# Optimization experiments

Hardware: AMD Instinct MI355X
Metric: run time of the kernel (lower is better)

## Reference

```python
import jax, jax.numpy as jnp
import numpy as np

H = 16  # n_heads


def _ln(x, g, b, eps=1e-5):
    m = x.mean(-1, keepdims=True)
    v = ((x - m) ** 2).mean(-1, keepdims=True)
    return (x - m) / jnp.sqrt(v + eps) * g + b


def setup_inputs() -> dict:
    key = jax.random.key(0)
    ks = jax.random.split(key, 10)
    b, lq, d, dff, L = 2, 1024, 1024, 4096, 4
    s = 0.02
    return {
        "x": jax.random.normal(ks[0], (b, lq, d), jnp.float32),
        "memory_bank": jax.random.normal(ks[1], (L, b, lq, d), jnp.float32),
        "attn_mask": jax.random.bernoulli(ks[2], 0.3, (b, lq, lq)),
        "ln1_g": jnp.ones((d,), jnp.float32),
        "ln1_b": jnp.zeros((d,), jnp.float32),
        "Wq": jax.random.normal(ks[3], (d, d), jnp.float32) * s,
        "Wk": jax.random.normal(ks[4], (d, d), jnp.float32) * s,
        "Wv": jax.random.normal(ks[5], (d, d), jnp.float32) * s,
        "Wo": jax.random.normal(ks[6], (d, d), jnp.float32) * s,
        "ln2_g": jnp.ones((d,), jnp.float32),
        "ln2_b": jnp.zeros((d,), jnp.float32),
        "W1": jax.random.normal(ks[7], (d, dff), jnp.float32) * s,
        "b1": jnp.zeros((dff,), jnp.float32),
        "W2": jax.random.normal(ks[8], (dff, d), jnp.float32) * s,
        "b2": jnp.zeros((d,), jnp.float32),
    }


def reference(x, memory_bank, attn_mask, ln1_g, ln1_b, Wq, Wk, Wv, Wo,
              ln2_g, ln2_b, W1, b1, W2, b2):
    # x: [b, lq, d]; memory_bank: [L, b, lk, d]; attn_mask: [b, lq, lk] bool (True = masked)
    b, lq, d = x.shape
    dh = d // H
    # preprocess_attn: LayerNorm (eval mode -> dropouts are identity)
    q = _ln(x, ln1_g, ln1_b)
    # grow memory bank with current normalized input
    mem = jnp.concatenate([memory_bank, q[None]], axis=0)  # [L+1, b, lk, d]
    L, _, lk, _ = mem.shape
    # projections (bias-free); key/value projected per layer then flattened over (L, lk)
    pq = (q @ Wq).reshape(b, lq, H, dh).transpose(0, 2, 1, 3) * (dh ** -0.5)  # [b,h,lq,dh]
    pk = (mem @ Wk).transpose(1, 0, 2, 3).reshape(b, L * lk, H, dh).transpose(0, 2, 1, 3)
    pv = (mem @ Wv).transpose(1, 0, 2, 3).reshape(b, L * lk, H, dh).transpose(0, 2, 1, 3)
    scores = jnp.einsum('bhqd,bhkd->bhqk', pq, pk)           # [b,h,lq,L*lk]
    scores = scores.reshape(b, H, lq, L, lk)
    scores = jnp.where(attn_mask[:, None, :, None, :], -jnp.inf, scores)
    attn = jax.nn.softmax(scores.reshape(b, H, lq, L * lk), axis=-1)
    ctx = jnp.einsum('bhqk,bhkd->bhqd', attn, pv)            # [b,h,lq,dh]
    ctx = ctx.transpose(0, 2, 1, 3).reshape(b, lq, d)
    attn_out = ctx @ Wo
    # postprocess_attn: residual add
    x2 = x + attn_out
    # FFN: LayerNorm -> Linear -> ReLU -> Linear -> residual
    f = _ln(x2, ln2_g, ln2_b)
    f = jax.nn.relu(f @ W1 + b1) @ W2 + b2
    out = x2 + f
    return (out, mem)
```

## Files before the change

### kernel.cpp

```cpp
#include <hip/hip_runtime.h>
#include <hip/hip_bf16.h>

typedef __attribute__((ext_vector_type(8))) __bf16 bf16x8;
typedef __attribute__((ext_vector_type(4))) __bf16 bf16x4;
typedef __attribute__((ext_vector_type(4))) float f32x4;

#define MFMA16(a, b, c) __builtin_amdgcn_mfma_f32_16x16x32_bf16((a), (b), (c), 0, 0, 0)
#define LOG2E 1.4426950408889634f

static __device__ __forceinline__ float exp2_fast(float x) {
    float r; asm("v_exp_f32 %0, %1" : "=v"(r) : "v"(x)); return r;
}

__device__ __forceinline__ void gll16(const void* g, void* l) {
    __builtin_amdgcn_global_load_lds((const __attribute__((address_space(1))) void*)g,
                                     (__attribute__((address_space(3))) void*)l,
                                     16, 0, 0);
}

__global__ __launch_bounds__(256) void prep_kernel(const float* __restrict__ bank,
                                                   float* __restrict__ mem_out,
                                                   __bf16* __restrict__ membf,
                                                   const float* __restrict__ x,
                                                   const float* __restrict__ g,
                                                   const float* __restrict__ bta,
                                                   float* __restrict__ q_out,
                                                   __bf16* __restrict__ qbf) {
    __shared__ float rs[4], rs2[4];
    int blk = blockIdx.x;
    if (blk < 2048) {
        int i = blk * 256 + threadIdx.x;
        const float4* i4 = (const float4*)bank;
        float4* o4 = (float4*)mem_out;
        for (; i < 2097152; i += 2048 * 256) {
            float4 v = i4[i];
            o4[i] = v;
            if (membf) {
                bf16x4 ob = {(__bf16)v.x, (__bf16)v.y, (__bf16)v.z, (__bf16)v.w};
                ((bf16x4*)membf)[i] = ob;
            }
        }
    } else {
        int row = blk - 2048;
        const float4 v = ((const float4*)(x + (size_t)row * 1024))[threadIdx.x];
        float s = v.x + v.y + v.z + v.w;
        float s2 = v.x * v.x + v.y * v.y + v.z * v.z + v.w * v.w;
#pragma unroll
        for (int off = 1; off < 64; off <<= 1) {
            s += __shfl_xor(s, off);
            s2 += __shfl_xor(s2, off);
        }
        int wv = threadIdx.x >> 6;
        if ((threadIdx.x & 63) == 0) { rs[wv] = s; rs2[wv] = s2; }
        __syncthreads();
        s = rs[0] + rs[1] + rs[2] + rs[3];
        s2 = rs2[0] + rs2[1] + rs2[2] + rs2[3];
        float mean = s * (1.0f / 1024.0f);
        float var = s2 * (1.0f / 1024.0f) - mean * mean;
        float rstd = rsqrtf(var + 1e-5f);
        float4 gg = ((const float4*)g)[threadIdx.x];
        float4 bb = ((const float4*)bta)[threadIdx.x];
        float4 o;
        o.x = (v.x - mean) * rstd * gg.x + bb.x;
        o.y = (v.y - mean) * rstd * gg.y + bb.y;
        o.z = (v.z - mean) * rstd * gg.z + bb.z;
        o.w = (v.w - mean) * rstd * gg.w + bb.w;
        ((float4*)(q_out + (size_t)row * 1024))[threadIdx.x] = o;
        if (qbf) {
            bf16x4 ob = {(__bf16)o.x, (__bf16)o.y, (__bf16)o.z, (__bf16)o.w};
            ((bf16x4*)(qbf + (size_t)row * 1024))[threadIdx.x] = ob;
        }
    }
}

__global__ __launch_bounds__(256) void ln_kernel(const float* __restrict__ x,
                                                 const float* __restrict__ g,
                                                 const float* __restrict__ bta,
                                                 __bf16* __restrict__ outb) {
    int row = blockIdx.x;
    const float4 v = ((const float4*)(x + (size_t)row * 1024))[threadIdx.x];
    float s = v.x + v.y + v.z + v.w;
    float s2 = v.x * v.x + v.y * v.y + v.z * v.z + v.w * v.w;
#pragma unroll
    for (int off = 1; off < 64; off <<= 1) {
        s += __shfl_xor(s, off);
        s2 += __shfl_xor(s2, off);
    }
    __shared__ float rs[4], rs2[4];
    int wv = threadIdx.x >> 6;
    if ((threadIdx.x & 63) == 0) { rs[wv] = s; rs2[wv] = s2; }
    __syncthreads();
    s = rs[0] + rs[1] + rs[2] + rs[3];
    s2 = rs2[0] + rs2[1] + rs2[2] + rs2[3];
    float mean = s * (1.0f / 1024.0f);
    float var = s2 * (1.0f / 1024.0f) - mean * mean;
    float rstd = rsqrtf(var + 1e-5f);
    float4 gg = ((const float4*)g)[threadIdx.x];
    float4 bb = ((const float4*)bta)[threadIdx.x];
    bf16x4 ob;
    ob[0] = (__bf16)((v.x - mean) * rstd * gg.x + bb.x);
    ob[1] = (__bf16)((v.y - mean) * rstd * gg.y + bb.y);
    ob[2] = (__bf16)((v.z - mean) * rstd * gg.z + bb.z);
    ob[3] = (__bf16)((v.w - mean) * rstd * gg.w + bb.w);
    ((bf16x4*)(outb + (size_t)row * 1024))[threadIdx.x] = ob;
}

__global__ __launch_bounds__(256) void comb_ln2(const float* __restrict__ pc0,
                                                const float* __restrict__ pc1,
                                                const float* __restrict__ x,
                                                const float* __restrict__ g,
                                                const float* __restrict__ bta,
                                                float* __restrict__ x2,
                                                __bf16* __restrict__ fln) {
    int row = blockIdx.x;
    int idx = row * 256 + threadIdx.x;
    float4 a = ((const float4*)pc0)[idx];
    float4 b = ((const float4*)pc1)[idx];
    float4 r = ((const float4*)x)[idx];
    float4 v;
    v.x = a.x + b.x + r.x;
    v.y = a.y + b.y + r.y;
    v.z = a.z + b.z + r.z;
    v.w = a.w + b.w + r.w;
    ((float4*)x2)[idx] = v;
    float s = v.x + v.y + v.z + v.w;
    float s2 = v.x * v.x + v.y * v.y + v.z * v.z + v.w * v.w;
#pragma unroll
    for (int off = 1; off < 64; off <<= 1) {
        s += __shfl_xor(s, off);
        s2 += __shfl_xor(s2, off);
    }
    __shared__ float rs[4], rs2[4];
    int wv = threadIdx.x >> 6;
    if ((threadIdx.x & 63) == 0) { rs[wv] = s; rs2[wv] = s2; }
    __syncthreads();
    s = rs[0] + rs[1] + rs[2] + rs[3];
    s2 = rs2[0] + rs2[1] + rs2[2] + rs2[3];
    float mean = s * (1.0f / 1024.0f);
    float var = s2 * (1.0f / 1024.0f) - mean * mean;
    float rstd = rsqrtf(var + 1e-5f);
    float4 gg = ((const float4*)g)[threadIdx.x];
    float4 bb = ((const float4*)bta)[threadIdx.x];
    bf16x4 ob;
    ob[0] = (__bf16)((v.x - mean) * rstd * gg.x + bb.x);
    ob[1] = (__bf16)((v.y - mean) * rstd * gg.y + bb.y);
    ob[2] = (__bf16)((v.z - mean) * rstd * gg.z + bb.z);
    ob[3] = (__bf16)((v.w - mean) * rstd * gg.w + bb.w);
    ((bf16x4*)(fln + (size_t)row * 1024))[threadIdx.x] = ob;
}

__device__ __forceinline__ void tr_body(const float* __restrict__ in, __bf16* __restrict__ out,
                                        int K, int N, int k0, int n0) {
    __shared__ float tile[32][33];
    int tx = threadIdx.x & 31, ty = threadIdx.x >> 5;
#pragma unroll
    for (int i = 0; i < 4; i++)
        tile[ty + i * 8][tx] = in[(size_t)(k0 + ty + i * 8) * N + n0 + tx];
    __syncthreads();
#pragma unroll
    for (int i = 0; i < 4; i++)
        out[(size_t)(n0 + ty + i * 8) * K + k0 + tx] = (__bf16)tile[tx][ty + i * 8];
}

__global__ __launch_bounds__(256) void tr_early(const float* __restrict__ Wq,
                                                const float* __restrict__ Wk,
                                                const float* __restrict__ Wv,
                                                __bf16* __restrict__ Wq_t,
                                                __bf16* __restrict__ Wkv_t) {
    int w = blockIdx.x;
    int sel = w >> 10, within = w & 1023;
    const float* in = (sel == 0) ? Wq : ((sel == 1) ? Wk : Wv);
    __bf16* out = (sel == 0) ? Wq_t : (Wkv_t + (size_t)(sel - 1) * 1048576);
    tr_body(in, out, 1024, 1024, (within >> 5) * 32, (within & 31) * 32);
}

__global__ __launch_bounds__(256) void tr_late(const float* __restrict__ Wo,
                                               const float* __restrict__ W1,
                                               const float* __restrict__ W2,
                                               __bf16* __restrict__ Wo_t,
                                               __bf16* __restrict__ W1_t,
                                               __bf16* __restrict__ W2_t) {
    int w = blockIdx.x;
    const float* in;
    __bf16* out;
    int K, N, k0, n0;
    if (w < 1024) {
        in = Wo; out = Wo_t; K = 1024; N = 1024; n0 = (w & 31) * 32; k0 = (w >> 5) * 32;
    } else if (w < 5120) {
        int v = w - 1024;
        in = W1; out = W1_t; K = 1024; N = 4096; n0 = (v & 127) * 32; k0 = (v >> 7) * 32;
    } else {
        int v = w - 5120;
        in = W2; out = W2_t; K = 4096; N = 1024; n0 = (v & 31) * 32; k0 = (v >> 5) * 32;
    }
    tr_body(in, out, K, N, k0, n0);
}

template <int EPI, bool ABF16>
__device__ __forceinline__ void gemm_core(const void* __restrict__ Av,
                                          const __bf16* __restrict__ Bt,
                                          void* __restrict__ Cout,
                                          const float* __restrict__ bias,
                                          const float* __restrict__ res,
                                          int N, int lda, int ldb, int klen,
                                          float scale, int bm, int bn) {
    constexpr int LDA = ABF16 ? 32 : 40;
    __shared__ __bf16 As[128 * LDA];
    __shared__ __bf16 Bs[128 * 32];

    int t = threadIdx.x;
    int lane = t & 63, wave = t >> 6;
    int wm = (wave >> 1) * 64, wn = (wave & 1) * 64;
    int l16 = lane & 15, l4 = lane >> 4;

    f32x4 acc[4][4];
#pragma unroll
    for (int m = 0; m < 4; m++)
#pragma unroll
        for (int n = 0; n < 4; n++) acc[m][n] = (f32x4){0.f, 0.f, 0.f, 0.f};

    int srow = t >> 2;
    int scol = (t & 3) * 8;
    int ar = t >> 1, ak = (t & 1) * 16;
    const __bf16* Ab = (const __bf16*)Av;
    const float* Af = (const float*)Av;

    for (int k0 = 0; k0 < klen; k0 += 32) {
        gll16(Bt + (size_t)(bn + srow) * ldb + (k0 + scol), &Bs[wave * 512]);
        gll16(Bt + (size_t)(bn + 64 + srow) * ldb + (k0 + scol), &Bs[2048 + wave * 512]);
        if constexpr (ABF16) {
            gll16(Ab + (size_t)(bm + srow) * lda + (k0 + scol), &As[wave * 512]);
            gll16(Ab + (size_t)(bm + 64 + srow) * lda + (k0 + scol), &As[2048 + wave * 512]);
        } else {
            const float* ap = Af + (size_t)(bm + ar) * lda + k0 + ak;
            float4 f0 = ((const float4*)ap)[0];
            float4 f1 = ((const float4*)ap)[1];
            float4 f2 = ((const float4*)ap)[2];
            float4 f3 = ((const float4*)ap)[3];
            float ta[16] = {f0.x, f0.y, f0.z, f0.w, f1.x, f1.y, f1.z, f1.w,
                            f2.x, f2.y, f2.z, f2.w, f3.x, f3.y, f3.z, f3.w};
            bf16x8 v0, v1;
#pragma unroll
            for (int j = 0; j < 8; j++) { v0[j] = (__bf16)ta[j]; v1[j] = (__bf16)ta[j + 8]; }
            *(bf16x8*)&As[ar * 40 + ak] = v0;
            *(bf16x8*)&As[ar * 40 + ak + 8] = v1;
        }
        __syncthreads();

        bf16x8 af[4], bfr[4];
#pragma unroll
        for (int m = 0; m < 4; m++) af[m] = *(const bf16x8*)&As[(wm + m * 16 + l16) * LDA + l4 * 8];
#pragma unroll
        for (int n = 0; n < 4; n++) bfr[n] = *(const bf16x8*)&Bs[(wn + n * 16 + l16) * 32 + l4 * 8];
#pragma unroll
        for (int m = 0; m < 4; m++)
#pragma unroll
            for (int n = 0; n < 4; n++) acc[m][n] = MFMA16(af[m], bfr[n], acc[m][n]);
        __syncthreads();
    }

#pragma unroll
    for (int m = 0; m < 4; m++) {
#pragma unroll
        for (int r = 0; r < 4; r++) {
            int row = bm + wm + m * 16 + l4 * 4 + r;
#pragma unroll
            for (int n = 0; n < 4; n++) {
                int col = bn + wn + n * 16 + l16;
                float c = acc[m][n][r];
                size_t idx = (size_t)row * N + col;
                if (EPI == 0) {
                    ((__bf16*)Cout)[idx] = (__bf16)(c * scale);
                } else if (EPI == 1) {
                    ((float*)Cout)[idx] = c + res[idx];
                } else if (EPI == 2) {
                    ((__bf16*)Cout)[idx] = (__bf16)fmaxf(c + bias[col], 0.0f);
                } else if (EPI == 3) {
                    ((float*)Cout)[idx] = c + bias[col] + res[idx];
                } else {
                    ((float*)Cout)[idx] = c;
                }
            }
        }
    }
}

template <int EPI, bool ABF16>
__global__ __launch_bounds__(256) void gemm_bt(const void* __restrict__ Av,
                                               const __bf16* __restrict__ Bt,
                                               void* __restrict__ Cout,
                                               const float* __restrict__ bias,
                                               const float* __restrict__ res,
                                               int N, int K, float scale, int nbx) {
    int q = gridDim.x >> 3;
    int swz = (blockIdx.x & 7) * q + (blockIdx.x >> 3);
    int bn = (swz % nbx) * 128;
    int bm = (swz / nbx) * 128;
    gemm_core<EPI, ABF16>(Av, Bt, Cout, bias, res, N, K, K, K, scale, bm, bn);
}

template <bool ABF16>
__global__ __launch_bounds__(256) void gemm_proj(const void* __restrict__ Akv,
                                                 const __bf16* __restrict__ Wkv_t,
                                                 __bf16* __restrict__ PKV,
                                                 const void* __restrict__ Aq,
                                                 const __bf16* __restrict__ Wq_t,
                                                 __bf16* __restrict__ Pq) {
    int q = gridDim.x >> 3;
    int swz = (blockIdx.x & 7) * q + (blockIdx.x >> 3);
    const void* A;
    const __bf16* B;
    __bf16* C;
    int N, bm, bn;
    float sc;
    if (swz < 1280) {
        A = Akv; B = Wkv_t; C = PKV; N = 2048; sc = 1.0f;
        bn = (swz & 15) * 128; bm = (swz >> 4) * 128;
    } else {
        int p = swz - 1280;
        A = Aq; B = Wq_t; C = Pq; N = 1024; sc = 0.125f * LOG2E;
        bn = (p & 7) * 128; bm = (p >> 3) * 128;
    }
    gemm_core<0, ABF16>(A, B, C, nullptr, nullptr, N, 1024, 1024, 1024, sc, bm, bn);
}

__global__ __launch_bounds__(256) void gemm_w2(const __bf16* __restrict__ h1,
                                               const __bf16* __restrict__ W2_t,
                                               float* __restrict__ pc0,
                                               float* __restrict__ pc1) {
    int q = gridDim.x >> 3;
    int swz = (blockIdx.x & 7) * q + (blockIdx.x >> 3);
    int half = swz >> 7;
    int p = swz & 127;
    int bn = (p & 7) * 128, bm = (p >> 3) * 128;
    int koff = half * 2048;
    gemm_core<4, true>(h1 + koff, W2_t + koff, half ? pc1 : pc0, nullptr, nullptr,
                       1024, 4096, 4096, 2048, 1.0f, bm, bn);
}

__global__ __launch_bounds__(256) void gemm_wo(const __bf16* __restrict__ ctx,
                                               const __bf16* __restrict__ Wo_t,
                                               float* __restrict__ pc0,
                                               float* __restrict__ pc1) {
    int q = gridDim.x >> 3;
    int swz = (blockIdx.x & 7) * q + (blockIdx.x >> 3);
    int half = swz >> 7;
    int p = swz & 127;
    int bn = (p & 7) * 128, bm = (p >> 3) * 128;
    int koff = half * 512;
    gemm_core<4, true>(ctx + koff, Wo_t + koff, half ? pc1 : pc0, nullptr, nullptr,
                       1024, 1024, 1024, 512, 1.0f, bm, bn);
}

__global__ __launch_bounds__(256) void comb_kernel(const float* __restrict__ pc0,
                                                   const float* __restrict__ pc1,
                                                   const float* __restrict__ bias,
                                                   const float* __restrict__ res,
                                                   float* __restrict__ out) {
    int i = blockIdx.x * 256 + threadIdx.x;
    float4 a = ((const float4*)pc0)[i];
    float4 b = ((const float4*)pc1)[i];
    float4 r = ((const float4*)res)[i];
    float4 o;
    o.x = a.x + b.x + r.x;
    o.y = a.y + b.y + r.y;
    o.z = a.z + b.z + r.z;
    o.w = a.w + b.w + r.w;
    if (bias) {
        float4 bb = ((const float4*)bias)[i & 255];
        o.x += bb.x; o.y += bb.y; o.z += bb.z; o.w += bb.w;
    }
    ((float4*)out)[i] = o;
}

#define CK 64
#define NCH4 20
__global__ __launch_bounds__(256, 5) void attn_part(const __bf16* __restrict__ Pq,
                                                    const __bf16* __restrict__ PKV,
                                                    const unsigned char* __restrict__ mask,
                                                    __bf16* __restrict__ pacc,
                                                    float* __restrict__ pl) {
    int bh = blockIdx.x;
    int b = bh >> 4, h = bh & 15;
    int rng = blockIdx.z;
    int wave = threadIdx.x >> 6, lane = threadIdx.x & 63;
    int l16 = lane & 15, l4 = lane >> 4;
    int q0 = blockIdx.y * 64 + wave * 16;

    __shared__ __bf16 Ks[64][72];
    __shared__ __bf16 Vt[64][72];
    __shared__ __bf16 Ps[4][16][72];

    const f32x4 fzero = {0.f, 0.f, 0.f, 0.f};

    bf16x8 qf[2];
    {
        const __bf16* pqrow = Pq + (size_t)(b * 1024 + q0 + l16) * 1024 + h * 64;
        qf[0] = *(const bf16x8*)(pqrow + l4 * 8);
        qf[1] = *(const bf16x8*)(pqrow + 32 + l4 * 8);
    }

    f32x4 accT[4];
#pragma unroll
    for (int n = 0; n < 4; n++) accT[n] = fzero;
    float lsum = 0.0f;

    const unsigned char* mrow_p = mask + (size_t)b * (1024u * 1024u) + (size_t)(q0 + l16) * 1024;

    int tl = threadIdx.x;
    int skey = tl >> 2;
    int sd0 = (tl & 3) << 4;
    int kgbase = rng * 1280;

    bf16x8 rk0, rk1, rv0, rv1;
    unsigned int mk[4], mkn[4];
    {
        int kg = kgbase + skey;
        int lidx = kg >> 10, i = kg & 1023;
        size_t off = ((size_t)(lidx * 2048 + b * 1024 + i) << 11) + h * 64 + sd0;
        rk0 = *(const bf16x8*)(PKV + off);
        rk1 = *(const bf16x8*)(PKV + off + 8);
        rv0 = *(const bf16x8*)(PKV + off + 1024);
        rv1 = *(const bf16x8*)(PKV + off + 1032);
        int kloc = kgbase & 1023;
#pragma unroll
        for (int tile = 0; tile < 4; tile++)
            mk[tile] = *(const unsigned int*)(mrow_p + kloc + tile * 16 + l4 * 4);
    }

    for (int t = 0; t < NCH4; t++) {
        *(bf16x8*)&Ks[skey][sd0] = rk0;
        *(bf16x8*)&Ks[skey][sd0 + 8] = rk1;
#pragma unroll
        for (int j = 0; j < 8; j++) {
            int row = sd0 + j;
            Vt[row][skey ^ ((row >> 3) << 3)] = rv0[j];
            int row2 = sd0 + 8 + j;
            Vt[row2][skey ^ ((row2 >> 3) << 3)] = rv1[j];
        }
        __syncthreads();

        if (t + 1 < NCH4) {
            int kg = kgbase + (t + 1) * CK + skey;
            int lidx = kg >> 10, i = kg & 1023;
            size_t off = ((size_t)(lidx * 2048 + b * 1024 + i) << 11) + h * 64 + sd0;
            rk0 = *(const bf16x8*)(PKV + off);
            rk1 = *(const bf16x8*)(PKV + off + 8);
            rv0 = *(const bf16x8*)(PKV + off + 1024);
            rv1 = *(const bf16x8*)(PKV + off + 1032);
            int kloc = (kgbase + (t + 1) * CK) & 1023;
#pragma unroll
            for (int tile = 0; tile < 4; tile++)
                mkn[tile] = *(const unsigned int*)(mrow_p + kloc + tile * 16 + l4 * 4);
        }

        f32x4 s[4];
        __builtin_amdgcn_s_setprio(1);
#pragma unroll
        for (int tile = 0; tile < 4; tile++) {
            bf16x8 ka = *(const bf16x8*)&Ks[tile * 16 + l16][l4 * 8];
            bf16x8 kb = *(const bf16x8*)&Ks[tile * 16 + l16][32 + l4 * 8];
            f32x4 sz = fzero;
            sz = MFMA16(ka, qf[0], sz);
            sz = MFMA16(kb, qf[1], sz);
            s[tile] = sz;
        }
        __builtin_amdgcn_s_setprio(0);

        float psum = 0.0f;
#pragma unroll
        for (int tile = 0; tile < 4; tile++) {
            bf16x4 pk_;
#pragma unroll
            for (int r = 0; r < 4; r++) {
                float e = exp2_fast(s[tile][r]);
                e = ((mk[tile] >> (r * 8)) & 255u) ? 0.0f : e;
                psum += e;
                pk_[r] = (__bf16)e;
            }
            *(bf16x4*)&Ps[wave][l16][tile * 16 + l4 * 4] = pk_;
        }
        lsum += psum;
#pragma unroll
        for (int tile = 0; tile < 4; tile++) mk[tile] = mkn[tile];

        __builtin_amdgcn_s_setprio(1);
#pragma unroll
        for (int kk = 0; kk < 2; kk++) {
            bf16x8 pf = *(const bf16x8*)&Ps[wave][l16][kk * 32 + l4 * 8];
#pragma unroll
            for (int n = 0; n < 4; n++) {
                int row = n * 16 + l16;
                int colblk = (kk * 32 + l4 * 8) ^ ((row >> 3) << 3);
                bf16x8 vf = *(const bf16x8*)&Vt[row][colblk];
                accT[n] = MFMA16(vf, pf, accT[n]);
            }
        }
        __builtin_amdgcn_s_setprio(0);
        __syncthreads();
    }

    lsum += __shfl_xor(lsum, 16);
    lsum += __shfl_xor(lsum, 32);

    size_t blk = ((size_t)(bh * 16 + blockIdx.y) * 4 + rng);
    __bf16* pa = pacc + blk * 4096 + (size_t)(wave * 16 + l16) * 64;
#pragma unroll
    for (int n = 0; n < 4; n++) {
        bf16x4 o;
#pragma unroll
        for (int r = 0; r < 4; r++) o[r] = (__bf16)accT[n][r];
        *(bf16x4*)&pa[n * 16 + l4 * 4] = o;
    }
    if (l4 == 0) pl[blk * 64 + wave * 16 + l16] = lsum;
}

__global__ __launch_bounds__(256) void attn_comb(const __bf16* __restrict__ pacc,
                                                 const float* __restrict__ pl,
                                                 __bf16* __restrict__ ctx) {
    int bh = blockIdx.x, qb = blockIdx.y;
    int b = bh >> 4, h = bh & 15;
    int q = threadIdx.x >> 2, d0 = (threadIdx.x & 3) * 16;
    float acc[16];
#pragma unroll
    for (int j = 0; j < 16; j++) acc[j] = 0.0f;
    float l = 0.0f;
    size_t blk0 = ((size_t)(bh * 16 + qb)) * 4;
#pragma unroll
    for (int rng = 0; rng < 4; rng++) {
        size_t base = (blk0 + rng) * 4096 + (size_t)q * 64 + d0;
        bf16x8 a0 = *(const bf16x8*)&pacc[base];
        bf16x8 a1 = *(const bf16x8*)&pacc[base + 8];
#pragma unroll
        for (int j = 0; j < 8; j++) {
            acc[j] += (float)a0[j];
            acc[8 + j] += (float)a1[j];
        }
        l += pl[(blk0 + rng) * 64 + q];
    }
    float inv = 1.0f / l;
    __bf16* crow = ctx + ((size_t)(b * 1024 + qb * 64 + q) << 10) + h * 64 + d0;
    bf16x8 o0, o1;
#pragma unroll
    for (int j = 0; j < 8; j++) {
        o0[j] = (__bf16)(acc[j] * inv);
        o1[j] = (__bf16)(acc[8 + j] * inv);
    }
    *(bf16x8*)crow = o0;
    *(bf16x8*)(crow + 8) = o1;
}

#define KHALF 2560
#define NCH 40
__global__ __launch_bounds__(512, 4) void attn_kernel(const __bf16* __restrict__ Pq,
                                                      const __bf16* __restrict__ PKV,
                                                      const unsigned char* __restrict__ mask,
                                                      __bf16* __restrict__ ctx) {
    int bh = blockIdx.x;
    int b = bh >> 4, h = bh & 15;
    int wave = threadIdx.x >> 6, lane = threadIdx.x & 63;
    int grp = wave >> 2, wv = wave & 3;
    int l16 = lane & 15, l4 = lane >> 4;
    int q0 = blockIdx.y * 64 + wv * 16;

    __shared__ __bf16 Ks[2][64][72];
    __shared__ __bf16 Vt[2][64][72];
    __shared__ __bf16 Ps[8][16][72];

    const f32x4 fzero = {0.f, 0.f, 0.f, 0.f};

    bf16x8 qf[2];
    {
        const __bf16* pqrow = Pq + (size_t)(b * 1024 + q0 + l16) * 1024 + h * 64;
        qf[0] = *(const bf16x8*)(pqrow + l4 * 8);
        qf[1] = *(const bf16x8*)(pqrow + 32 + l4 * 8);
    }

    f32x4 accT[4];
#pragma unroll
    for (int n = 0; n < 4; n++) accT[n] = fzero;
    float lsum = 0.0f;

    const unsigned char* mrow_p = mask + (size_t)b * (1024u * 1024u) + (size_t)(q0 + l16) * 1024;

    int tl = threadIdx.x & 255;
    int skey = tl >> 2;
    int sd0 = (tl & 3) << 4;
    int kgbase = grp * KHALF;

    bf16x8 rk0, rk1, rv0, rv1;
    unsigned int mk[4], mkn[4];
    {
        int kg = kgbase + skey;
        int lidx = kg >> 10, i = kg & 1023;
        size_t off = ((size_t)(lidx * 2048 + b * 1024 + i) << 11) + h * 64 + sd0;
        rk0 = *(const bf16x8*)(PKV + off);
        rk1 = *(const bf16x8*)(PKV + off + 8);
        rv0 = *(const bf16x8*)(PKV + off + 1024);
        rv1 = *(const bf16x8*)(PKV + off + 1032);
        int kloc = kgbase & 1023;
#pragma unroll
        for (int tile = 0; tile < 4; tile++)
            mk[tile] = *(const unsigned int*)(mrow_p + kloc + tile * 16 + l4 * 4);
    }

    for (int t = 0; t < NCH; t++) {
        *(bf16x8*)&Ks[grp][skey][sd0] = rk0;
        *(bf16x8*)&Ks[grp][skey][sd0 + 8] = rk1;
#pragma unroll
        for (int j = 0; j < 8; j++) {
            int row = sd0 + j;
            Vt[grp][row][skey ^ ((row >> 3) << 3)] = rv0[j];
            int row2 = sd0 + 8 + j;
            Vt[grp][row2][skey ^ ((row2 >> 3) << 3)] = rv1[j];
        }
        __syncthreads();

        if (t + 1 < NCH) {
            int kg = kgbase + (t + 1) * CK + skey;
            int lidx = kg >> 10, i = kg & 1023;
            size_t off = ((size_t)(lidx * 2048 + b * 1024 + i) << 11) + h * 64 + sd0;
            rk0 = *(const bf16x8*)(PKV + off);
            rk1 = *(const bf16x8*)(PKV + off + 8);
            rv0 = *(const bf16x8*)(PKV + off + 1024);
            rv1 = *(const bf16x8*)(PKV + off + 1032);
            int kloc = (kgbase + (t + 1) * CK) & 1023;
#pragma unroll
            for (int tile = 0; tile < 4; tile++)
                mkn[tile] = *(const unsigned int*)(mrow_p + kloc + tile * 16 + l4 * 4);
        }

        f32x4 s[4];
        __builtin_amdgcn_s_setprio(1);
#pragma unroll
        for (int tile = 0; tile < 4; tile++) {
            bf16x8 ka = *(const bf16x8*)&Ks[grp][tile * 16 + l16][l4 * 8];
            bf16x8 kb = *(const bf16x8*)&Ks[grp][tile * 16 + l16][32 + l4 * 8];
            f32x4 sz = fzero;
            sz = MFMA16(ka, qf[0], sz);
            sz = MFMA16(kb, qf[1], sz);
            s[tile] = sz;
        }
        __builtin_amdgcn_s_setprio(0);

        float psum = 0.0f;
#pragma unroll
        for (int tile = 0; tile < 4; tile++) {
            bf16x4 pk_;
#pragma unroll
            for (int r = 0; r < 4; r++) {
                float e = exp2_fast(s[tile][r]);
                e = ((mk[tile] >> (r * 8)) & 255u) ? 0.0f : e;
                psum += e;
                pk_[r] = (__bf16)e;
            }
            *(bf16x4*)&Ps[wave][l16][tile * 16 + l4 * 4] = pk_;
        }
        lsum += psum;
#pragma unroll
        for (int tile = 0; tile < 4; tile++) mk[tile] = mkn[tile];

        __builtin_amdgcn_s_setprio(1);
#pragma unroll
        for (int kk = 0; kk < 2; kk++) {
            bf16x8 pf = *(const bf16x8*)&Ps[wave][l16][kk * 32 + l4 * 8];
#pragma unroll
            for (int n = 0; n < 4; n++) {
                int row = n * 16 + l16;
                int colblk = (kk * 32 + l4 * 8) ^ ((row >> 3) << 3);
                bf16x8 vf = *(const bf16x8*)&Vt[grp][row][colblk];
                accT[n] = MFMA16(vf, pf, accT[n]);
            }
        }
        __builtin_amdgcn_s_setprio(0);
        __syncthreads();
    }

    lsum += __shfl_xor(lsum, 16);
    lsum += __shfl_xor(lsum, 32);

    float* exAcc = (float*)&Ks[0][0][0];
    float* exL = (float*)&Vt[0][0][0];
    if (grp == 1) {
#pragma unroll
        for (int n = 0; n < 4; n++)
            *(f32x4*)&exAcc[(wv * 16 + l16) * 68 + n * 16 + l4 * 4] = accT[n];
        if (l4 == 0) exL[wv * 16 + l16] = lsum;
    }
    __syncthreads();
    if (grp == 0) {
        int qi = wv * 16 + l16;
        float inv = 1.0f / (lsum + exL[qi]);
        __bf16* crow = ctx + ((size_t)(b * 1024 + q0 + l16) << 10) + h * 64;
#pragma unroll
        for (int n = 0; n < 4; n++) {
            f32x4 a1 = *(const f32x4*)&exAcc[qi * 68 + n * 16 + l4 * 4];
            bf16x4 o;
#pragma unroll
            for (int r = 0; r < 4; r++) o[r] = (__bf16)((accT[n][r] + a1[r]) * inv);
            *(bf16x4*)&crow[n * 16 + l4 * 4] = o;
        }
    }
}

extern "C" void kernel_launch(void* const* d_in, const int* in_sizes, int n_in,
                              void* d_out, int out_size, void* d_ws, size_t ws_size,
                              hipStream_t stream) {
    const float* x = (const float*)d_in[0];
    const float* memory_bank = (const float*)d_in[1];
    const unsigned char* attn_mask = (const unsigned char*)d_in[2];
    const float* ln1_g = (const float*)d_in[3];
    const float* ln1_b = (const float*)d_in[4];
    const float* Wq = (const float*)d_in[5];
    const float* Wk = (const float*)d_in[6];
    const float* Wv = (const float*)d_in[7];
    const float* Wo = (const float*)d_in[8];
    const float* ln2_g = (const float*)d_in[9];
    const float* ln2_b = (const float*)d_in[10];
    const float* W1 = (const float*)d_in[11];
    const float* b1 = (const float*)d_in[12];
    const float* W2 = (const float*)d_in[13];
    const float* b2 = (const float*)d_in[14];

    float* out = (float*)d_out;
    float* mem_out = out + 2097152;
    float* q_out = mem_out + 4 * 2097152;

    char* ws = (char*)d_ws;
    bool big = ws_size >= (70ull << 20);

    __bf16* PKV = (__bf16*)ws;
    __bf16 *Pq, *Wq_t, *Wkv_t, *ctx, *membf = nullptr, *qbf = nullptr;
    __bf16* pacc = nullptr;
    float* plv = nullptr;
    if (big) {
        membf = (__bf16*)(ws + (40ull << 20));
        qbf = membf + (size_t)8192 * 1024;
        Wq_t = (__bf16*)(ws + (60ull << 20));
        Wkv_t = (__bf16*)(ws + (62ull << 20));
        Pq = (__bf16*)(ws + (66ull << 20));
        ctx = (__bf16*)(ws + (60ull << 20));
        pacc = (__bf16*)(ws + (40ull << 20));
        plv = (float*)(ws + (56ull << 20));
    } else {
        Pq = (__bf16*)(ws + (40ull << 20));
        Wq_t = (__bf16*)(ws + (44ull << 20));
        Wkv_t = (__bf16*)(ws + (46ull << 20));
        ctx = (__bf16*)(ws + (44ull << 20));
    }
    __bf16* Wo_t = (__bf16*)ws;
    __bf16* W1_t = (__bf16*)(ws + (2ull << 20));
    __bf16* W2_t = (__bf16*)(ws + (10ull << 20));
    float* x2 = (float*)(ws + (18ull << 20));
    __bf16* fln = (__bf16*)(ws + (26ull << 20));
    __bf16* h1 = (__bf16*)(ws + (30ull << 20));
    float* wo_pc0 = (float*)(ws + (30ull << 20));
    float* wo_pc1 = (float*)(ws + (38ull << 20));
    float* pc0 = (float*)(ws + (46ull << 20));
    float* pc1 = (float*)(ws + (54ull << 20));

    prep_kernel<<<4096, 256, 0, stream>>>(memory_bank, mem_out, membf, x, ln1_g, ln1_b,
                                          q_out, qbf);
    tr_early<<<3072, 256, 0, stream>>>(Wq, Wk, Wv, Wq_t, Wkv_t);

    if (big)
        gemm_proj<true><<<1408, 256, 0, stream>>>(membf, Wkv_t, PKV, qbf, Wq_t, Pq);
    else
        gemm_proj<false><<<1408, 256, 0, stream>>>(mem_out, Wkv_t, PKV, q_out, Wq_t, Pq);

    if (big) {
        attn_part<<<dim3(32, 16, 4), 256, 0, stream>>>(Pq, PKV, attn_mask, pacc, plv);
        attn_comb<<<dim3(32, 16), 256, 0, stream>>>(pacc, plv, ctx);
    } else {
        attn_kernel<<<dim3(32, 16), 512, 0, stream>>>(Pq, PKV, attn_mask, ctx);
    }

    tr_late<<<9216, 256, 0, stream>>>(Wo, W1, W2, Wo_t, W1_t, W2_t);

    if (big) {
        gemm_wo<<<256, 256, 0, stream>>>(ctx, Wo_t, wo_pc0, wo_pc1);
        comb_ln2<<<2048, 256, 0, stream>>>(wo_pc0, wo_pc1, x, ln2_g, ln2_b, x2, fln);
    } else {
        gemm_bt<1, true><<<128, 256, 0, stream>>>(ctx, Wo_t, x2, nullptr, x, 1024, 1024, 1.0f, 8);
        ln_kernel<<<2048, 256, 0, stream>>>(x2, ln2_g, ln2_b, fln);
    }
    gemm_bt<2, true><<<512, 256, 0, stream>>>(fln, W1_t, h1, b1, nullptr, 4096, 1024, 1.0f, 32);
    if (big) {
        gemm_w2<<<256, 256, 0, stream>>>(h1, W2_t, pc0, pc1);
        comb_kernel<<<2048, 256, 0, stream>>>(pc0, pc1, b2, x2, out);
    } else {
        gemm_bt<3, true><<<128, 256, 0, stream>>>(h1, W2_t, out, b2, x2, 1024, 4096, 1.0f, 8);
    }
}
```

Measured before the change: 302.5 us.

## Switch split-K attention to 32x32 MFMA tiles with 128-query blocks and XOR swizzle

```diff
diff --git a/kernel.cpp b/kernel.cpp
--- a/kernel.cpp
+++ b/kernel.cpp
@@ -4,8 +4,10 @@
 typedef __attribute__((ext_vector_type(8))) __bf16 bf16x8;
 typedef __attribute__((ext_vector_type(4))) __bf16 bf16x4;
 typedef __attribute__((ext_vector_type(4))) float f32x4;
+typedef __attribute__((ext_vector_type(16))) float f32x16;
 
 #define MFMA16(a, b, c) __builtin_amdgcn_mfma_f32_16x16x32_bf16((a), (b), (c), 0, 0, 0)
+#define MFMA32(a, b, c) __builtin_amdgcn_mfma_f32_32x32x16_bf16((a), (b), (c), 0, 0, 0)
 #define LOG2E 1.4426950408889634f
 
 static __device__ __forceinline__ float exp2_fast(float x) {
@@ -373,9 +375,7 @@
     ((float4*)out)[i] = o;
 }
 
-#define CK 64
-#define NCH4 20
-__global__ __launch_bounds__(256, 5) void attn_part(const __bf16* __restrict__ Pq,
+__global__ __launch_bounds__(256, 3) void attn_part(const __bf16* __restrict__ Pq,
                                                     const __bf16* __restrict__ PKV,
                                                     const unsigned char* __restrict__ mask,
                                                     __bf16* __restrict__ pacc,
@@ -384,36 +384,50 @@
     int b = bh >> 4, h = bh & 15;
     int rng = blockIdx.z;
     int wave = threadIdx.x >> 6, lane = threadIdx.x & 63;
-    int l16 = lane & 15, l4 = lane >> 4;
-    int q0 = blockIdx.y * 64 + wave * 16;
-
-    __shared__ __bf16 Ks[64][72];
-    __shared__ __bf16 Vt[64][72];
-    __shared__ __bf16 Ps[4][16][72];
-
-    const f32x4 fzero = {0.f, 0.f, 0.f, 0.f};
-
-    bf16x8 qf[2];
+    int l32 = lane & 31, hi = lane >> 5;
+    int q0 = blockIdx.y * 128 + wave * 32;
+
+    __shared__ __bf16 Ks[64][64];
+    __shared__ __bf16 Vt[64][64];
+    __shared__ __bf16 Ps[4][32][64];
+
+    bf16x8 qf[4];
     {
-        const __bf16* pqrow = Pq + (size_t)(b * 1024 + q0 + l16) * 1024 + h * 64;
-        qf[0] = *(const bf16x8*)(pqrow + l4 * 8);
-        qf[1] = *(const bf16x8*)(pqrow + 32 + l4 * 8);
-    }
-
-    f32x4 accT[4];
-#pragma unroll
-    for (int n = 0; n < 4; n++) accT[n] = fzero;
+        const __bf16* pqrow = Pq + (size_t)(b * 1024 + q0 + l32) * 1024 + h * 64 + hi * 8;
+#pragma unroll
+        for (int ds = 0; ds < 4; ds++) qf[ds] = *(const bf16x8*)(pqrow + ds * 16);
+    }
+
+    f32x16 acc0, acc1;
+#pragma unroll
+    for (int i = 0; i < 16; i++) { acc0[i] = 0.f; acc1[i] = 0.f; }
     float lsum = 0.0f;
 
-    const unsigned char* mrow_p = mask + (size_t)b * (1024u * 1024u) + (size_t)(q0 + l16) * 1024;
+    const unsigned char* mrow_p = mask + (size_t)b * (1024u * 1024u)
+                                  + (size_t)(q0 + l32) * 1024 + hi * 4;
 
     int tl = threadIdx.x;
     int skey = tl >> 2;
     int sd0 = (tl & 3) << 4;
     int kgbase = rng * 1280;
 
+    int Gq = (l32 ^ (l32 >> 3)) & 7;
+    int Gk = (skey ^ (skey >> 3)) & 7;
+    int kw0 = skey * 64 + ((((sd0 >> 3) + 0) ^ Gk) << 3);
+    int kw1 = skey * 64 + ((((sd0 >> 3) + 1) ^ Gk) << 3);
+    int vwa[16];
+#pragma unroll
+    for (int j = 0; j < 16; j++) {
+        int row = sd0 + j;
+        int Gr = (row ^ (row >> 3)) & 7;
+        vwa[j] = row * 64 + ((((skey >> 3) ^ Gr) << 3) | (skey & 7));
+    }
+    __bf16* KsF = &Ks[0][0];
+    __bf16* VtF = &Vt[0][0];
+    __bf16* PsF = &Ps[wave][0][0];
+
     bf16x8 rk0, rk1, rv0, rv1;
-    unsigned int mk[4], mkn[4];
+    unsigned int mk[8], mkn[8];
     {
         int kg = kgbase + skey;
         int lidx = kg >> 10, i = kg & 1023;
@@ -424,98 +438,104 @@
         rv1 = *(const bf16x8*)(PKV + off + 1032);
         int kloc = kgbase & 1023;
 #pragma unroll
-        for (int tile = 0; tile < 4; tile++)
-            mk[tile] = *(const unsigned int*)(mrow_p + kloc + tile * 16 + l4 * 4);
-    }
-
-    for (int t = 0; t < NCH4; t++) {
-        *(bf16x8*)&Ks[skey][sd0] = rk0;
-        *(bf16x8*)&Ks[skey][sd0 + 8] = rk1;
-#pragma unroll
-        for (int j = 0; j < 8; j++) {
-            int row = sd0 + j;
-            Vt[row][skey ^ ((row >> 3) << 3)] = rv0[j];
-            int row2 = sd0 + 8 + j;
-            Vt[row2][skey ^ ((row2 >> 3) << 3)] = rv1[j];
-        }
+        for (int d = 0; d < 8; d++)
+            mk[d] = *(const unsigned int*)(mrow_p + kloc + (d >> 2) * 32 + (d & 3) * 8);
+    }
+
+    for (int t = 0; t < 20; t++) {
+        *(bf16x8*)&KsF[kw0] = rk0;
+        *(bf16x8*)&KsF[kw1] = rk1;
+#pragma unroll
+        for (int j = 0; j < 8; j++) { VtF[vwa[j]] = rv0[j]; VtF[vwa[j + 8]] = rv1[j]; }
         __syncthreads();
 
-        if (t + 1 < NCH4) {
-            int kg = kgbase + (t + 1) * CK + skey;
+        if (t + 1 < 20) {
+            int kg = kgbase + (t + 1) * 64 + skey;
             int lidx = kg >> 10, i = kg & 1023;
             size_t off = ((size_t)(lidx * 2048 + b * 1024 + i) << 11) + h * 64 + sd0;
             rk0 = *(const bf16x8*)(PKV + off);
             rk1 = *(const bf16x8*)(PKV + off + 8);
             rv0 = *(const bf16x8*)(PKV + off + 1024);
             rv1 = *(const bf16x8*)(PKV + off + 1032);
-            int kloc = (kgbase + (t + 1) * CK) & 1023;
-#pragma unroll
-            for (int tile = 0; tile < 4; tile++)
-                mkn[tile] = *(const unsigned int*)(mrow_p + kloc + tile * 16 + l4 * 4);
-        }
-
-        f32x4 s[4];
+            int kloc = (kgbase + (t + 1) * 64) & 1023;
+#pragma unroll
+            for (int d = 0; d < 8; d++)
+                mkn[d] = *(const unsigned int*)(mrow_p + kloc + (d >> 2) * 32 + (d & 3) * 8);
+        }
+
+        float psum = 0.0f;
+#pragma unroll
+        for (int kb = 0; kb < 2; kb++) {
+            f32x16 s;
+#pragma unroll
+            for (int i = 0; i < 16; i++) s[i] = 0.f;
+            __builtin_amdgcn_s_setprio(1);
+#pragma unroll
+            for (int ds = 0; ds < 4; ds++) {
+                int row = kb * 32 + l32;
+                int Gr = (row ^ (row >> 3)) & 7;
+                bf16x8 ka = *(const bf16x8*)&KsF[row * 64 + (((ds * 2 + hi) ^ Gr) << 3)];
+                s = MFMA32(ka, qf[ds], s);
+            }
+            __builtin_amdgcn_s_setprio(0);
+#pragma unroll
+            for (int g = 0; g < 4; g++) {
+                bf16x4 pk_;
+                unsigned int mkd = mk[kb * 4 + g];
+#pragma unroll
+                for (int m = 0; m < 4; m++) {
+                    float e = exp2_fast(s[g * 4 + m]);
+                    e = ((mkd >> (m * 8)) & 255u) ? 0.0f : e;
+                    psum += e;
+                    pk_[m] = (__bf16)e;
+                }
+                *(bf16x4*)&PsF[l32 * 64 + ((((kb * 4 + g) ^ Gq) << 3) | (hi * 4))] = pk_;
+            }
+        }
+        lsum += psum;
+#pragma unroll
+        for (int d = 0; d < 8; d++) mk[d] = mkn[d];
+
         __builtin_amdgcn_s_setprio(1);
 #pragma unroll
-        for (int tile = 0; tile < 4; tile++) {
-            bf16x8 ka = *(const bf16x8*)&Ks[tile * 16 + l16][l4 * 8];
-            bf16x8 kb = *(const bf16x8*)&Ks[tile * 16 + l16][32 + l4 * 8];
-            f32x4 sz = fzero;
-            sz = MFMA16(ka, qf[0], sz);
-            sz = MFMA16(kb, qf[1], sz);
-            s[tile] = sz;
-        }
-        __builtin_amdgcn_s_setprio(0);
-
-        float psum = 0.0f;
-#pragma unroll
-        for (int tile = 0; tile < 4; tile++) {
-            bf16x4 pk_;
-#pragma unroll
-            for (int r = 0; r < 4; r++) {
-                float e = exp2_fast(s[tile][r]);
-                e = ((mk[tile] >> (r * 8)) & 255u) ? 0.0f : e;
-                psum += e;
-                pk_[r] = (__bf16)e;
+        for (int ks = 0; ks < 4; ks++) {
+            bf16x8 pf = *(const bf16x8*)&PsF[l32 * 64 + (((ks * 2 + hi) ^ Gq) << 3)];
+            {
+                int row = l32;
+                int Gr = (row ^ (row >> 3)) & 7;
+                bf16x8 vf = *(const bf16x8*)&VtF[row * 64 + (((ks * 2 + hi) ^ Gr) << 3)];
+                acc0 = MFMA32(vf, pf, acc0);
             }
-            *(bf16x4*)&Ps[wave][l16][tile * 16 + l4 * 4] = pk_;
-        }
-        lsum += psum;
-#pragma unroll
-        for (int tile = 0; tile < 4; tile++) mk[tile] = mkn[tile];
-
-        __builtin_amdgcn_s_setprio(1);
-#pragma unroll
-        for (int kk = 0; kk < 2; kk++) {
-            bf16x8 pf = *(const bf16x8*)&Ps[wave][l16][kk * 32 + l4 * 8];
-#pragma unroll
-            for (int n = 0; n < 4; n++) {
-                int row = n * 16 + l16;
-                int colblk = (kk * 32 + l4 * 8) ^ ((row >> 3) << 3);
-                bf16x8 vf = *(const bf16x8*)&Vt[row][colblk];
-                accT[n] = MFMA16(vf, pf, accT[n]);
+            {
+                int row = 32 + l32;
+                int Gr = (row ^ (row >> 3)) & 7;
+                bf16x8 vf = *(const bf16x8*)&VtF[row * 64 + (((ks * 2 + hi) ^ Gr) << 3)];
+                acc1 = MFMA32(vf, pf, acc1);
             }
         }
         __builtin_amdgcn_s_setprio(0);
         __syncthreads();
     }
 
-    lsum += __shfl_xor(lsum, 16);
     lsum += __shfl_xor(lsum, 32);
 
-    size_t blk = ((size_t)(bh * 16 + blockIdx.y) * 4 + rng);
-    __bf16* pa = pacc + blk * 4096 + (size_t)(wave * 16 + l16) * 64;
-#pragma unroll
-    for (int n = 0; n < 4; n++) {
-        bf16x4 o;
-#pragma unroll
-        for (int r = 0; r < 4; r++) o[r] = (__bf16)accT[n][r];
-        *(bf16x4*)&pa[n * 16 + l4 * 4] = o;
-    }
-    if (l4 == 0) pl[blk * 64 + wave * 16 + l16] = lsum;
-}
-
-__global__ __launch_bounds__(256) void attn_comb(const __bf16* __restrict__ pacc,
+    size_t blk = ((size_t)(bh * 8 + blockIdx.y) * 4 + rng);
+    __bf16* pa = pacc + blk * 8192 + (size_t)(wave * 32 + l32) * 64;
+#pragma unroll
+    for (int g = 0; g < 4; g++) {
+        bf16x4 o0, o1;
+#pragma unroll
+        for (int m = 0; m < 4; m++) {
+            o0[m] = (__bf16)acc0[g * 4 + m];
+            o1[m] = (__bf16)acc1[g * 4 + m];
+        }
+        *(bf16x4*)&pa[g * 8 + hi * 4] = o0;
+        *(bf16x4*)&pa[32 + g * 8 + hi * 4] = o1;
+    }
+    if (hi == 0) pl[blk * 128 + wave * 32 + l32] = lsum;
+}
+
+__global__ __launch_bounds__(512) void attn_comb(const __bf16* __restrict__ pacc,
                                                  const float* __restrict__ pl,
                                                  __bf16* __restrict__ ctx) {
     int bh = blockIdx.x, qb = blockIdx.y;
@@ -525,10 +545,10 @@
 #pragma unroll
     for (int j = 0; j < 16; j++) acc[j] = 0.0f;
     float l = 0.0f;
-    size_t blk0 = ((size_t)(bh * 16 + qb)) * 4;
+    size_t blk0 = ((size_t)(bh * 8 + qb)) * 4;
 #pragma unroll
     for (int rng = 0; rng < 4; rng++) {
-        size_t base = (blk0 + rng) * 4096 + (size_t)q * 64 + d0;
+        size_t base = (blk0 + rng) * 8192 + (size_t)q * 64 + d0;
         bf16x8 a0 = *(const bf16x8*)&pacc[base];
         bf16x8 a1 = *(const bf16x8*)&pacc[base + 8];
 #pragma unroll
@@ -536,10 +556,10 @@
             acc[j] += (float)a0[j];
             acc[8 + j] += (float)a1[j];
         }
-        l += pl[(blk0 + rng) * 64 + q];
+        l += pl[(blk0 + rng) * 128 + q];
     }
     float inv = 1.0f / l;
-    __bf16* crow = ctx + ((size_t)(b * 1024 + qb * 64 + q) << 10) + h * 64 + d0;
+    __bf16* crow = ctx + ((size_t)(b * 1024 + qb * 128 + q) << 10) + h * 64 + d0;
     bf16x8 o0, o1;
 #pragma unroll
     for (int j = 0; j < 8; j++) {
@@ -551,6 +571,7 @@
 }
 
 #define KHALF 2560
+#define CK 64
 #define NCH 40
 __global__ __launch_bounds__(512, 4) void attn_kernel(const __bf16* __restrict__ Pq,
                                                       const __bf16* __restrict__ PKV,
@@ -769,8 +790,8 @@
         gemm_proj<false><<<1408, 256, 0, stream>>>(mem_out, Wkv_t, PKV, q_out, Wq_t, Pq);
 
     if (big) {
-        attn_part<<<dim3(32, 16, 4), 256, 0, stream>>>(Pq, PKV, attn_mask, pacc, plv);
-        attn_comb<<<dim3(32, 16), 256, 0, stream>>>(pacc, plv, ctx);
+        attn_part<<<dim3(32, 8, 4), 256, 0, stream>>>(Pq, PKV, attn_mask, pacc, plv);
+        attn_comb<<<dim3(32, 8), 512, 0, stream>>>(pacc, plv, ctx);
     } else {
         attn_kernel<<<dim3(32, 16), 512, 0, stream>>>(Pq, PKV, attn_mask, ctx);
     }
```

Result: faster. 293.4 us (-3.0%).
